# Kernel tuning notes

Hardware: AMD Instinct MI355X
Metric: run time of the kernel (lower is better)

Reference implementation:

```python
import jax, jax.numpy as jnp
import numpy as np

EPS = 1e-6

def rms_norm(x):
    # RMSNorm over last dim, no learned weight (torch F.rms_norm without weight)
    return x * jax.lax.rsqrt(jnp.mean(jnp.square(x), axis=-1, keepdims=True) + EPS)

def apply_rotary_emb(x, cos, sin):
    # x: [b, t, h, d]; cos/sin: [t, d//2] -> broadcast [1, t, 1, d//2]
    half = x.shape[-1] // 2
    c = cos[None, :, None, :]
    s = sin[None, :, None, :]
    x1, x2 = x[..., :half], x[..., half:]
    return jnp.concatenate([x1 * c - x2 * s, x2 * c + x1 * s], axis=-1)

def setup_inputs() -> dict:
    key = jax.random.key(0)
    ks = jax.random.split(key, 16)
    B, T, E, H = 4, 2048, 1024, 16
    D = E // H
    inp = {
        "query": jax.random.normal(ks[0], (B, T, E), jnp.float32),
        "key": jax.random.normal(ks[1], (B, T, E), jnp.float32),
        "value": jax.random.normal(ks[2], (B, T, E), jnp.float32),
        "attn_mask": jnp.tril(jnp.ones((T, T), dtype=bool)),
        "cos": jnp.cos(jnp.arange(T)[:, None] / (10000.0 ** (jnp.arange(D // 2) / (D // 2)))[None, :]).astype(jnp.float32),
        "sin": jnp.sin(jnp.arange(T)[:, None] / (10000.0 ** (jnp.arange(D // 2) / (D // 2)))[None, :]).astype(jnp.float32),
        "Wq": jax.random.normal(ks[3], (E, E), jnp.float32) * 0.02,
        "bq": jnp.zeros((E,), jnp.float32),
        "Wk": jax.random.normal(ks[4], (E, E), jnp.float32) * 0.02,
        "bk": jnp.zeros((E,), jnp.float32),
        "Wv": jax.random.normal(ks[5], (E, E), jnp.float32) * 0.02,
        "bv": jnp.zeros((E,), jnp.float32),
        "Wo": jax.random.normal(ks[6], (E, E), jnp.float32) * 0.02,
        "bo": jnp.zeros((E,), jnp.float32),
    }
    return inp

def reference(query, key, value, attn_mask, cos, sin, Wq, bq, Wk, bk, Wv, bv, Wo, bo):
    B, T, E = query.shape
    H = 16
    D = E // H
    q = query @ Wq.T + bq
    k = key @ Wk.T + bk
    v = value @ Wv.T + bv
    q = q.reshape(B, T, H, D)
    k = k.reshape(B, T, H, D)
    v = v.reshape(B, T, H, D)
    q, k = rms_norm(q), rms_norm(k)
    q = apply_rotary_emb(q, cos, sin)
    k = apply_rotary_emb(k, cos, sin)
    # SDPA: [b, h, t, d] layout via einsum directly from [b, t, h, d]
    scale = 1.0 / jnp.sqrt(jnp.float32(D))
    scores = jnp.einsum('bqhd,bkhd->bhqk', q, k) * scale
    scores = jnp.where(attn_mask[None, None, :, :], scores, jnp.float32(-jnp.inf))
    attn = jax.nn.softmax(scores, axis=-1)
    o = jnp.einsum('bhqk,bkhd->bqhd', attn, v).reshape(B, T, E)
    return o @ Wo.T + bo
```

## Files before the change

### kernel.cpp

```cpp
#include <hip/hip_runtime.h>

typedef __bf16 bf16;
typedef __bf16 bf16x8 __attribute__((ext_vector_type(8)));
typedef __bf16 bf16x4 __attribute__((ext_vector_type(4)));
typedef float  floatx4 __attribute__((ext_vector_type(4)));

#define B_ 4
#define T_ 2048
#define E_ 1024
#define H_ 16
#define D_ 64
#define NTE_ (B_ * T_ * E_)

#define NEG_BIG (-1e30f)
#define SMAX2 12.2629081f

#define OFF_CQ 0ull
#define OFF_CK ((unsigned long long)NTE_)
#define OFF_CV (2ull * NTE_)
#define OFF_WQ (3ull * NTE_)
#define OFF_WK (OFF_WQ + 1048576ull)
#define OFF_WV (OFF_WK + 1048576ull)
#define OFF_WO (OFF_WV + 1048576ull)
__device__ bf16 g_conv[3ull * NTE_ + 4ull * 1048576ull];
__device__ bf16 g_scratch[4ull * NTE_];

__device__ __forceinline__ floatx4 mfma16(bf16x8 a, bf16x8 b, floatx4 c) {
  return __builtin_amdgcn_mfma_f32_16x16x32_bf16(a, b, c, 0, 0, 0);
}

__device__ __forceinline__ void async_copy16(void* lds, const void* g) {
  __builtin_amdgcn_global_load_lds(
      (const __attribute__((address_space(1))) unsigned int*)g,
      (__attribute__((address_space(3))) unsigned int*)lds, 16, 0, 0);
}

__global__ __launch_bounds__(256) void convert_all(const float4* __restrict__ q,
                                                   const float4* __restrict__ k,
                                                   const float4* __restrict__ v,
                                                   const float4* __restrict__ wq,
                                                   const float4* __restrict__ wk,
                                                   const float4* __restrict__ wv,
                                                   const float4* __restrict__ wo) {
  const float4* srcs[7] = {q, k, v, wq, wk, wv, wo};
  bf16x4* dsts[7] = {(bf16x4*)(g_conv + OFF_CQ), (bf16x4*)(g_conv + OFF_CK),
                     (bf16x4*)(g_conv + OFF_CV), (bf16x4*)(g_conv + OFF_WQ),
                     (bf16x4*)(g_conv + OFF_WK), (bf16x4*)(g_conv + OFF_WV),
                     (bf16x4*)(g_conv + OFF_WO)};
  const int n4s[7] = {NTE_ / 4, NTE_ / 4, NTE_ / 4, 262144, 262144, 262144, 262144};
  int i0 = blockIdx.x * 256 + threadIdx.x;
  int stride = gridDim.x * 256;
#pragma unroll
  for (int s = 0; s < 7; ++s) {
    const float4* sp = srcs[s];
    bf16x4* dp = dsts[s];
    int n4 = n4s[s];
    for (int i = i0; i < n4; i += stride) {
      float4 vv = sp[i];
      bf16x4 o;
      o[0] = (bf16)vv.x; o[1] = (bf16)vv.y; o[2] = (bf16)vv.z; o[3] = (bf16)vv.w;
      dp[i] = o;
    }
  }
}

template <int EPI>
__device__ __forceinline__ void gemm_epilogue(floatx4 (&acc)[4][4],
                                              const float* __restrict__ bias,
                                              void* __restrict__ Yv, int M0, int N0,
                                              int wm, int wn, int q, int r,
                                              const float* __restrict__ cosb,
                                              const float* __restrict__ sinb) {
  float bcol[4];
#pragma unroll
  for (int ni = 0; ni < 4; ++ni) bcol[ni] = bias[N0 + wn + ni * 16 + r];

  if (EPI == 0 || EPI == 1) {
    const float post = (EPI == 0) ? 0.18033688f : 1.0f;
    bf16* Y = (bf16*)Yv;
#pragma unroll
    for (int mi = 0; mi < 4; ++mi) {
      const int rowbase = M0 + wm + mi * 16 + q * 4;
#pragma unroll
      for (int rr = 0; rr < 4; ++rr) {
        const int row = rowbase + rr;
        const int ts = row & (T_ - 1);
        float v0 = acc[mi][0][rr] + bcol[0];
        float v1 = acc[mi][1][rr] + bcol[1];
        float v2 = acc[mi][2][rr] + bcol[2];
        float v3 = acc[mi][3][rr] + bcol[3];
        float ss = v0 * v0 + v1 * v1 + v2 * v2 + v3 * v3;
        ss += __shfl_xor(ss, 1, 64);
        ss += __shfl_xor(ss, 2, 64);
        ss += __shfl_xor(ss, 4, 64);
        ss += __shfl_xor(ss, 8, 64);
        const float rs = rsqrtf(ss * (1.0f / 64.0f) + 1e-6f);
        const float y0 = v0 * rs, y1 = v1 * rs, y2 = v2 * rs, y3 = v3 * rs;
        const float c0 = cosb[ts * 32 + r], s0 = sinb[ts * 32 + r];
        const float c1 = cosb[ts * 32 + 16 + r], s1 = sinb[ts * 32 + 16 + r];
        bf16 o0 = (bf16)((y0 * c0 - y2 * s0) * post);
        bf16 o1 = (bf16)((y1 * c1 - y3 * s1) * post);
        bf16 o2 = (bf16)((y2 * c0 + y0 * s0) * post);
        bf16 o3 = (bf16)((y3 * c1 + y1 * s1) * post);
        bf16* yp = Y + (size_t)row * 1024 + N0 + wn + r;
        yp[0] = o0; yp[16] = o1; yp[32] = o2; yp[48] = o3;
      }
    }
  } else if (EPI == 2) {
    bf16* Y = (bf16*)Yv;
#pragma unroll
    for (int mi = 0; mi < 4; ++mi) {
      const int rowbase = M0 + wm + mi * 16 + q * 4;
      const int bb = rowbase >> 11;
      const int t0 = rowbase & (T_ - 1);
#pragma unroll
      for (int ni = 0; ni < 4; ++ni) {
        const int col = N0 + wn + ni * 16 + r;
        const int head = col >> 6;
        const int d = col & 63;
        bf16x4 pk;
#pragma unroll
        for (int rr = 0; rr < 4; ++rr) pk[rr] = (bf16)(acc[mi][ni][rr] + bcol[ni]);
        *(bf16x4*)(Y + ((size_t)(bb * 16 + head) * 64 + d) * 2048 + t0) = pk;
      }
    }
  } else {
    float* Y = (float*)Yv;
#pragma unroll
    for (int mi = 0; mi < 4; ++mi) {
      const int rowbase = M0 + wm + mi * 16 + q * 4;
#pragma unroll
      for (int ni = 0; ni < 4; ++ni) {
        const int col = N0 + wn + ni * 16 + r;
#pragma unroll
        for (int rr = 0; rr < 4; ++rr)
          Y[(size_t)(rowbase + rr) * 1024 + col] = acc[mi][ni][rr] + bcol[ni];
      }
    }
  }
}

template <int EPI>
__device__ __forceinline__ void gemm_core(char* __restrict__ smem,
                                          const bf16* __restrict__ X,
                                          const bf16* __restrict__ W,
                                          const float* __restrict__ bias,
                                          void* __restrict__ Yv, int M0, int N0,
                                          const float* __restrict__ cosb,
                                          const float* __restrict__ sinb) {
  constexpr int NT = 16;

  const int tid = threadIdx.x;
  const int w = tid >> 6;
  const int l = tid & 63;
  const int q = l >> 4;
  const int r = l & 15;
  const int lrow = l >> 3;
  const int rs7 = r & 7;
  const int wm = (w >> 2) * 64;
  const int wn = (w & 3) * 64;
  const int colb = ((l & 7) ^ lrow) << 4;
  const int sl0 = ((0 + q) ^ rs7) << 4;
  const int sl1 = ((4 + q) ^ rs7) << 4;

  char* const Ab = smem;
  char* const Bb = smem + 49152;
  const int aoff = (wm + r) * 128;
  const int boff = (wn + r) * 128;

  const char* gA = (const char*)X + (size_t)(M0 + w * 16 + lrow) * 2048 + colb;
  const char* gB = (const char*)W + (size_t)(N0 + w * 32 + lrow) * 2048 + colb;

  floatx4 acc[4][4];
#pragma unroll
  for (int mi = 0; mi < 4; ++mi)
#pragma unroll
    for (int ni = 0; ni < 4; ++ni) acc[mi][ni] = (floatx4){0.f, 0.f, 0.f, 0.f};

#define STA(bi, t)                                             \
  do {                                                         \
    char* d_ = Ab + (bi) * 16384 + w * 2048;                   \
    const char* s_ = gA + (size_t)(t) * 128;                   \
    async_copy16(d_, s_);                                      \
    async_copy16(d_ + 1024, s_ + 16384);                       \
  } while (0)
#define STB(bi, t)                                             \
  do {                                                         \
    char* d_ = Bb + (bi) * 32768 + w * 4096;                   \
    const char* s_ = gB + (size_t)(t) * 128;                   \
    async_copy16(d_, s_);                                      \
    async_copy16(d_ + 1024, s_ + 16384);                       \
    async_copy16(d_ + 2048, s_ + 32768);                       \
    async_copy16(d_ + 3072, s_ + 49152);                       \
  } while (0)

  STB(0, 0); STA(0, 0);
  STB(1, 1); STA(1, 1);
  STB(2, 2); STA(2, 2);
  asm volatile("s_waitcnt vmcnt(12)" ::: "memory");
  asm volatile("s_barrier" ::: "memory");

#pragma unroll
  for (int t = 0; t < NT; ++t) {
    const int ib = t % 3;
    const int st = (t + 2) % 3;

    if (t >= 1 && t + 2 < NT) { STB(st, t + 2); STA(st, t + 2); }

    const char* rA = Ab + ib * 16384;
    const char* rB = Bb + ib * 32768;

    bf16x8 af[4][2], bv[4][2];
#pragma unroll
    for (int mi = 0; mi < 4; ++mi) {
      af[mi][0] = *(const bf16x8*)(rA + aoff + mi * 2048 + sl0);
      af[mi][1] = *(const bf16x8*)(rA + aoff + mi * 2048 + sl1);
    }
#pragma unroll
    for (int ni = 0; ni < 4; ++ni) {
      bv[ni][0] = *(const bf16x8*)(rB + boff + ni * 2048 + sl0);
      bv[ni][1] = *(const bf16x8*)(rB + boff + ni * 2048 + sl1);
    }
#pragma unroll
    for (int mi = 0; mi < 4; ++mi)
#pragma unroll
      for (int ni = 0; ni < 4; ++ni) {
        acc[mi][ni] = mfma16(af[mi][0], bv[ni][0], acc[mi][ni]);
        acc[mi][ni] = mfma16(af[mi][1], bv[ni][1], acc[mi][ni]);
      }

    if (t + 3 <= NT) {
      asm volatile("s_waitcnt vmcnt(6)" ::: "memory");
    } else if (t + 2 == NT) {
      asm volatile("s_waitcnt vmcnt(0)" ::: "memory");
    }
    if (t + 1 < NT) asm volatile("s_barrier" ::: "memory");
  }
#undef STA
#undef STB

  gemm_epilogue<EPI>(acc, bias, Yv, M0, N0, wm, wn, q, r, cosb, sinb);
}

__global__ __launch_bounds__(512, 1) void gemm_qkv(const float* __restrict__ bq,
                                                   const float* __restrict__ bk,
                                                   const float* __restrict__ bv,
                                                   const float* __restrict__ cosb,
                                                   const float* __restrict__ sinb) {
  __shared__ __align__(16) char smem[147456];
  int bid = blockIdx.x;
  int s = (bid & 7) * 96 + (bid >> 3);
  int z = s >> 8;
  int rem = s & 255;
  int mt = rem >> 2, nt = rem & 3;
  const bf16* X = g_conv + OFF_CQ + (unsigned long long)z * NTE_;
  const bf16* W = g_conv + OFF_WQ + (unsigned long long)z * 1048576ull;
  if (z == 0) {
    gemm_core<0>(smem, X, W, bq, (void*)g_scratch, mt * 128, nt * 256, cosb, sinb);
  } else if (z == 1) {
    gemm_core<1>(smem, X, W, bk, (void*)(g_scratch + (unsigned long long)NTE_),
                 mt * 128, nt * 256, cosb, sinb);
  } else {
    gemm_core<2>(smem, X, W, bv, (void*)(g_scratch + 2ull * NTE_),
                 mt * 128, nt * 256, nullptr, nullptr);
  }
}

__global__ __launch_bounds__(512, 1) void gemm_out(const bf16* __restrict__ X,
                                                   const bf16* __restrict__ W,
                                                   const float* __restrict__ bias,
                                                   float* __restrict__ Y) {
  __shared__ __align__(16) char smem[147456];
  int bid = blockIdx.x;
  int s = (bid & 7) * 32 + (bid >> 3);
  int mt = s >> 2, nt = s & 3;
  gemm_core<3>(smem, X, W, bias, (void*)Y, mt * 128, nt * 256, nullptr, nullptr);
}

#define KSTR 72
#define PSTR 72
__global__ __launch_bounds__(256, 4) void flash_attn() {
  const bf16* qp = g_scratch;
  const bf16* kp = g_scratch + (unsigned long long)NTE_;
  const bf16* vt = g_scratch + 2ull * NTE_;
  bf16* op = g_scratch + 3ull * NTE_;

  __shared__ __align__(16) bf16 sK[64 * KSTR];
  __shared__ __align__(16) bf16 sV[64 * KSTR];
  __shared__ __align__(16) bf16 sP[4 * 32 * PSTR];

  const int bid = blockIdx.x;
  const int xcd = bid & 7;
  const int lb = bid >> 3;
  const int bh = xcd * 8 + (lb & 7);
  const int qt = 15 - (lb >> 3);
  const int h = bh & 15, b = bh >> 4;
  const int tid = threadIdx.x, w = tid >> 6, l = tid & 63, g = l >> 4, r = l & 15;
  const int Q0 = qt * 128;
  const int qw = Q0 + w * 32;

  const bf16* kbase = kp + (size_t)(b * T_) * E_ + h * D_;
  const bf16* vbase = vt + (size_t)bh * D_ * T_;
  bf16* pw = sP + w * (32 * PSTR);

  bf16x8 ones;
#pragma unroll
  for (int i = 0; i < 8; ++i) ones[i] = (bf16)1.0f;

  bf16x8 qa[2][2];
#pragma unroll
  for (int qb = 0; qb < 2; ++qb)
#pragma unroll
    for (int hf = 0; hf < 2; ++hf)
      qa[qb][hf] = *(const bf16x8*)(qp + (size_t)(b * T_ + qw + qb * 16 + r) * E_ +
                                    h * D_ + hf * 32 + g * 8);

  floatx4 o_acc[2][4], l_acc[2];
#pragma unroll
  for (int qb = 0; qb < 2; ++qb) {
    l_acc[qb] = (floatx4){0.f, 0.f, 0.f, 0.f};
#pragma unroll
    for (int dt = 0; dt < 4; ++dt) o_acc[qb][dt] = (floatx4){0.f, 0.f, 0.f, 0.f};
  }

  int srow[2], scc[2];
#pragma unroll
  for (int i = 0; i < 2; ++i) {
    int idx = i * 256 + tid;
    srow[i] = idx >> 3;
    scc[i] = (idx & 7) * 8;
  }

  bf16x8 kreg[2], vreg[2];
#pragma unroll
  for (int i = 0; i < 2; ++i) {
    kreg[i] = *(const bf16x8*)(kbase + (size_t)srow[i] * E_ + scc[i]);
    vreg[i] = *(const bf16x8*)(vbase + (size_t)srow[i] * T_ + scc[i]);
  }

  const int lastKt = Q0 + 64;
  for (int kt0 = 0; kt0 <= lastKt; kt0 += 64) {
    __syncthreads();
#pragma unroll
    for (int i = 0; i < 2; ++i) {
      *(bf16x8*)(sK + srow[i] * KSTR + scc[i]) = kreg[i];
      *(bf16x8*)(sV + srow[i] * KSTR + scc[i]) = vreg[i];
    }
    if (kt0 < lastKt) {
      int kt1 = kt0 + 64;
#pragma unroll
      for (int i = 0; i < 2; ++i) {
        kreg[i] = *(const bf16x8*)(kbase + (size_t)(kt1 + srow[i]) * E_ + scc[i]);
        vreg[i] = *(const bf16x8*)(vbase + (size_t)srow[i] * T_ + kt1 + scc[i]);
      }
    }
    __syncthreads();

    if (kt0 <= qw + 31) {
      const bool needMask = (kt0 + 63 > qw);

#pragma unroll
      for (int sc = 0; sc < 4; ++sc) {
        bf16x8 kb0 = *(const bf16x8*)(sK + (sc * 16 + r) * KSTR + g * 8);
        bf16x8 kb1 = *(const bf16x8*)(sK + (sc * 16 + r) * KSTR + 32 + g * 8);
        floatx4 s0 = (floatx4){0.f, 0.f, 0.f, 0.f};
        floatx4 s1 = (floatx4){0.f, 0.f, 0.f, 0.f};
        s0 = mfma16(kb0, qa[0][0], s0);
        s0 = mfma16(kb1, qa[0][1], s0);
        s1 = mfma16(kb0, qa[1][0], s1);
        s1 = mfma16(kb1, qa[1][1], s1);

        if (needMask) {
          int kg = kt0 + sc * 16 + g * 4;
          int qg0 = qw + r;
          int qg1 = qw + 16 + r;
#pragma unroll
          for (int rr = 0; rr < 4; ++rr) {
            if (kg + rr > qg0) s0[rr] = NEG_BIG;
            if (kg + rr > qg1) s1[rr] = NEG_BIG;
          }
        }

        bf16x4 p0, p1;
#pragma unroll
        for (int rr = 0; rr < 4; ++rr) {
          p0[rr] = (bf16)exp2f(s0[rr] - SMAX2);
          p1[rr] = (bf16)exp2f(s1[rr] - SMAX2);
        }
        *(bf16x4*)(pw + r * PSTR + sc * 16 + g * 4) = p0;
        *(bf16x4*)(pw + (16 + r) * PSTR + sc * 16 + g * 4) = p1;
      }

#pragma unroll
      for (int kk = 0; kk < 2; ++kk) {
        bf16x8 vb[4];
#pragma unroll
        for (int dt = 0; dt < 4; ++dt)
          vb[dt] = *(const bf16x8*)(sV + (dt * 16 + r) * KSTR + kk * 32 + g * 8);
#pragma unroll
        for (int qb = 0; qb < 2; ++qb) {
          bf16x8 pa = *(const bf16x8*)(pw + (qb * 16 + r) * PSTR + kk * 32 + g * 8);
          l_acc[qb] = mfma16(pa, ones, l_acc[qb]);
#pragma unroll
          for (int dt = 0; dt < 4; ++dt)
            o_acc[qb][dt] = mfma16(pa, vb[dt], o_acc[qb][dt]);
        }
      }
    }
  }

  float linv[2][4];
#pragma unroll
  for (int qb = 0; qb < 2; ++qb)
#pragma unroll
    for (int rr = 0; rr < 4; ++rr) linv[qb][rr] = 1.0f / l_acc[qb][rr];
#pragma unroll
  for (int qb = 0; qb < 2; ++qb)
#pragma unroll
    for (int dt = 0; dt < 4; ++dt)
#pragma unroll
      for (int rr = 0; rr < 4; ++rr) {
        int t = qw + qb * 16 + g * 4 + rr;
        op[(size_t)(b * T_ + t) * E_ + h * D_ + dt * 16 + r] =
            (bf16)(o_acc[qb][dt][rr] * linv[qb][rr]);
      }
}

extern "C" void kernel_launch(void* const* d_in, const int* in_sizes, int n_in,
                              void* d_out, int out_size, void* d_ws, size_t ws_size,
                              hipStream_t stream) {
  float* out = (float*)d_out;

  void* cvp_ = nullptr;
  void* sp_ = nullptr;
  (void)hipGetSymbolAddress(&cvp_, HIP_SYMBOL(g_conv));
  (void)hipGetSymbolAddress(&sp_, HIP_SYMBOL(g_scratch));
  bf16* cv = (bf16*)cvp_;
  bf16* sc = (bf16*)sp_;

  const float* cosb = (const float*)d_in[4];
  const float* sinb = (const float*)d_in[5];
  const float* bq = (const float*)d_in[7];
  const float* bk = (const float*)d_in[9];
  const float* bv = (const float*)d_in[11];
  const float* bo = (const float*)d_in[13];

  convert_all<<<dim3(1024), dim3(256), 0, stream>>>(
      (const float4*)d_in[0], (const float4*)d_in[1], (const float4*)d_in[2],
      (const float4*)d_in[6], (const float4*)d_in[8], (const float4*)d_in[10],
      (const float4*)d_in[12]);

  bf16* op = sc + 3ull * NTE_;

  gemm_qkv<<<dim3(768), dim3(512), 0, stream>>>(bq, bk, bv, cosb, sinb);
  flash_attn<<<dim3(1024), dim3(256), 0, stream>>>();
  gemm_out<<<dim3(256), dim3(512), 0, stream>>>(op, cv + OFF_WO, bo, out);
}
```

Before: 333.1 us.

## Double flash-attention query tile to 256 rows and balance causal tile order

Each flash-attention block now handles 256 query rows instead of 128, with each wave owning 64 rows, so every K/V tile loaded into shared memory is reused across twice as many queries. The grid is halved to 512 blocks, and query tiles are issued in an interleaved long/short order to balance the causal workload. The cost is more accumulator registers and a larger P buffer in shared memory, which lowers occupancy (launch bounds drop from 4 to 2 blocks). Diagonal tiles also waste more masked work.

```diff
diff --git a/kernel.cpp b/kernel.cpp
--- a/kernel.cpp
+++ b/kernel.cpp
@@ -279,7 +279,7 @@
 
 #define KSTR 72
 #define PSTR 72
-__global__ __launch_bounds__(256, 4) void flash_attn() {
+__global__ __launch_bounds__(256, 2) void flash_attn() {
   const bf16* qp = g_scratch;
   const bf16* kp = g_scratch + (unsigned long long)NTE_;
   const bf16* vt = g_scratch + 2ull * NTE_;
@@ -287,37 +287,38 @@
 
   __shared__ __align__(16) bf16 sK[64 * KSTR];
   __shared__ __align__(16) bf16 sV[64 * KSTR];
-  __shared__ __align__(16) bf16 sP[4 * 32 * PSTR];
+  __shared__ __align__(16) bf16 sP[4 * 64 * PSTR];
 
   const int bid = blockIdx.x;
   const int xcd = bid & 7;
   const int lb = bid >> 3;
   const int bh = xcd * 8 + (lb & 7);
-  const int qt = 15 - (lb >> 3);
+  constexpr int qord[8] = {7, 0, 6, 1, 5, 2, 4, 3};
+  const int qt = qord[lb >> 3];
   const int h = bh & 15, b = bh >> 4;
   const int tid = threadIdx.x, w = tid >> 6, l = tid & 63, g = l >> 4, r = l & 15;
-  const int Q0 = qt * 128;
-  const int qw = Q0 + w * 32;
+  const int Q0 = qt * 256;
+  const int qw = Q0 + w * 64;
 
   const bf16* kbase = kp + (size_t)(b * T_) * E_ + h * D_;
   const bf16* vbase = vt + (size_t)bh * D_ * T_;
-  bf16* pw = sP + w * (32 * PSTR);
+  bf16* pw = sP + w * (64 * PSTR);
 
   bf16x8 ones;
 #pragma unroll
   for (int i = 0; i < 8; ++i) ones[i] = (bf16)1.0f;
 
-  bf16x8 qa[2][2];
-#pragma unroll
-  for (int qb = 0; qb < 2; ++qb)
+  bf16x8 qa[4][2];
+#pragma unroll
+  for (int qb = 0; qb < 4; ++qb)
 #pragma unroll
     for (int hf = 0; hf < 2; ++hf)
       qa[qb][hf] = *(const bf16x8*)(qp + (size_t)(b * T_ + qw + qb * 16 + r) * E_ +
                                     h * D_ + hf * 32 + g * 8);
 
-  floatx4 o_acc[2][4], l_acc[2];
-#pragma unroll
-  for (int qb = 0; qb < 2; ++qb) {
+  floatx4 o_acc[4][4], l_acc[4];
+#pragma unroll
+  for (int qb = 0; qb < 4; ++qb) {
     l_acc[qb] = (floatx4){0.f, 0.f, 0.f, 0.f};
 #pragma unroll
     for (int dt = 0; dt < 4; ++dt) o_acc[qb][dt] = (floatx4){0.f, 0.f, 0.f, 0.f};
@@ -338,7 +339,7 @@
     vreg[i] = *(const bf16x8*)(vbase + (size_t)srow[i] * T_ + scc[i]);
   }
 
-  const int lastKt = Q0 + 64;
+  const int lastKt = Q0 + 192;
   for (int kt0 = 0; kt0 <= lastKt; kt0 += 64) {
     __syncthreads();
 #pragma unroll
@@ -356,39 +357,40 @@
     }
     __syncthreads();
 
-    if (kt0 <= qw + 31) {
+    if (kt0 <= qw + 63) {
       const bool needMask = (kt0 + 63 > qw);
 
 #pragma unroll
       for (int sc = 0; sc < 4; ++sc) {
         bf16x8 kb0 = *(const bf16x8*)(sK + (sc * 16 + r) * KSTR + g * 8);
         bf16x8 kb1 = *(const bf16x8*)(sK + (sc * 16 + r) * KSTR + 32 + g * 8);
-        floatx4 s0 = (floatx4){0.f, 0.f, 0.f, 0.f};
-        floatx4 s1 = (floatx4){0.f, 0.f, 0.f, 0.f};
-        s0 = mfma16(kb0, qa[0][0], s0);
-        s0 = mfma16(kb1, qa[0][1], s0);
-        s1 = mfma16(kb0, qa[1][0], s1);
-        s1 = mfma16(kb1, qa[1][1], s1);
+        floatx4 s[4];
+#pragma unroll
+        for (int qb = 0; qb < 4; ++qb) {
+          floatx4 a = (floatx4){0.f, 0.f, 0.f, 0.f};
+          a = mfma16(kb0, qa[qb][0], a);
+          a = mfma16(kb1, qa[qb][1], a);
+          s[qb] = a;
+        }
 
         if (needMask) {
           int kg = kt0 + sc * 16 + g * 4;
-          int qg0 = qw + r;
-          int qg1 = qw + 16 + r;
-#pragma unroll
-          for (int rr = 0; rr < 4; ++rr) {
-            if (kg + rr > qg0) s0[rr] = NEG_BIG;
-            if (kg + rr > qg1) s1[rr] = NEG_BIG;
+#pragma unroll
+          for (int qb = 0; qb < 4; ++qb) {
+            int qg = qw + qb * 16 + r;
+#pragma unroll
+            for (int rr = 0; rr < 4; ++rr)
+              if (kg + rr > qg) s[qb][rr] = NEG_BIG;
           }
         }
 
-        bf16x4 p0, p1;
-#pragma unroll
-        for (int rr = 0; rr < 4; ++rr) {
-          p0[rr] = (bf16)exp2f(s0[rr] - SMAX2);
-          p1[rr] = (bf16)exp2f(s1[rr] - SMAX2);
+#pragma unroll
+        for (int qb = 0; qb < 4; ++qb) {
+          bf16x4 p;
+#pragma unroll
+          for (int rr = 0; rr < 4; ++rr) p[rr] = (bf16)exp2f(s[qb][rr] - SMAX2);
+          *(bf16x4*)(pw + (qb * 16 + r) * PSTR + sc * 16 + g * 4) = p;
         }
-        *(bf16x4*)(pw + r * PSTR + sc * 16 + g * 4) = p0;
-        *(bf16x4*)(pw + (16 + r) * PSTR + sc * 16 + g * 4) = p1;
       }
 
 #pragma unroll
@@ -398,7 +400,7 @@
         for (int dt = 0; dt < 4; ++dt)
           vb[dt] = *(const bf16x8*)(sV + (dt * 16 + r) * KSTR + kk * 32 + g * 8);
 #pragma unroll
-        for (int qb = 0; qb < 2; ++qb) {
+        for (int qb = 0; qb < 4; ++qb) {
           bf16x8 pa = *(const bf16x8*)(pw + (qb * 16 + r) * PSTR + kk * 32 + g * 8);
           l_acc[qb] = mfma16(pa, ones, l_acc[qb]);
 #pragma unroll
@@ -409,13 +411,13 @@
     }
   }
 
-  float linv[2][4];
-#pragma unroll
-  for (int qb = 0; qb < 2; ++qb)
+  float linv[4][4];
+#pragma unroll
+  for (int qb = 0; qb < 4; ++qb)
 #pragma unroll
     for (int rr = 0; rr < 4; ++rr) linv[qb][rr] = 1.0f / l_acc[qb][rr];
 #pragma unroll
-  for (int qb = 0; qb < 2; ++qb)
+  for (int qb = 0; qb < 4; ++qb)
 #pragma unroll
     for (int dt = 0; dt < 4; ++dt)
 #pragma unroll
@@ -453,6 +455,6 @@
   bf16* op = sc + 3ull * NTE_;
 
   gemm_qkv<<<dim3(768), dim3(512), 0, stream>>>(bq, bk, bv, cosb, sinb);
-  flash_attn<<<dim3(1024), dim3(256), 0, stream>>>();
+  flash_attn<<<dim3(512), dim3(256), 0, stream>>>();
   gemm_out<<<dim3(256), dim3(512), 0, stream>>>(op, cv + OFF_WO, bo, out);
 }
```

Result: slower. 350.2 us (+5.2%).
